# Kernel tuning notes

Measured on AMD Instinct MI355X. Metric: run time of the kernel, lower is better.

Reference implementation:

```python
import jax, jax.numpy as jnp
import numpy as np
from jax import lax

B, L, N = 512, 128, 64      # batch, data_len//2, numOfSmart
H = 16                      # conv channels == lstm hidden
PW = (N - 3) // 2           # pooled width = 30
FEAT = H * PW               # lstm input = 480
BN_EPS = 1e-5


def setup_inputs() -> dict:
    key = jax.random.key(0)
    ks = jax.random.split(key, 24)
    rn = lambda k, shape, s=0.05: jax.random.normal(k, shape, dtype=jnp.float32) * s
    return {
        "input1": jax.random.normal(ks[0], (B, L, N), dtype=jnp.float32),
        "input2": jax.random.normal(ks[1], (B, L, N), dtype=jnp.float32),
        "w_x_q": rn(ks[2], (N, N), 0.1),
        "w_x_k": rn(ks[3], (L, 1), 0.1),
        "w_y_q": rn(ks[4], (L, L), 0.1),
        "w_y_k": rn(ks[5], (1, N), 0.1),
        "pos_emb": rn(ks[6], (L, N), 0.1),
        "conv_w": rn(ks[7], (H, 1, 1, 4), 0.2),
        "conv_b": rn(ks[8], (H,), 0.1),
        "bn_gamma": jnp.ones((H,), jnp.float32),
        "bn_beta": jnp.zeros((H,), jnp.float32),
        "bn_mean": jnp.zeros((H,), jnp.float32),
        "bn_var": jnp.ones((H,), jnp.float32),
        "lstm_Wih0": rn(ks[9], (4 * H, FEAT)),
        "lstm_Whh0": rn(ks[10], (4 * H, H)),
        "lstm_bih0": rn(ks[11], (4 * H,)),
        "lstm_bhh0": rn(ks[12], (4 * H,)),
        "lstm_Wih1": rn(ks[13], (4 * H, H)),
        "lstm_Whh1": rn(ks[14], (4 * H, H)),
        "lstm_bih1": rn(ks[15], (4 * H,)),
        "lstm_bhh1": rn(ks[16], (4 * H,)),
        "fc1_w": rn(ks[17], (8 * L, 16 * L), 0.02),
        "fc1_b": rn(ks[18], (8 * L,), 0.02),
        "fc2_w": rn(ks[19], (8 * L, 8 * L), 0.02),
        "fc2_b": rn(ks[20], (8 * L,), 0.02),
        "fc3_w": rn(ks[21], (20, 8 * L), 0.02),
        "fc3_b": rn(ks[22], (20,), 0.02),
    }


def _lstm_layer(xs, Wih, Whh, bih, bhh):
    # xs: [T, Bt, F]; torch gate order i, f, g, o
    Bt = xs.shape[1]
    h0 = jnp.zeros((Bt, Whh.shape[1]), xs.dtype)

    def step(carry, xt):
        h, c = carry
        g = xt @ Wih.T + h @ Whh.T + bih + bhh
        i, f, gg, o = jnp.split(g, 4, axis=-1)
        c = jax.nn.sigmoid(f) * c + jax.nn.sigmoid(i) * jnp.tanh(gg)
        h = jax.nn.sigmoid(o) * jnp.tanh(c)
        return (h, c), h

    _, ys = lax.scan(step, (h0, h0), xs)
    return ys


def reference(input1, input2, w_x_q, w_x_k, w_y_q, w_y_k, pos_emb, conv_w, conv_b,
              bn_gamma, bn_beta, bn_mean, bn_var,
              lstm_Wih0, lstm_Whh0, lstm_bih0, lstm_bhh0,
              lstm_Wih1, lstm_Whh1, lstm_bih1, lstm_bhh1,
              fc1_w, fc1_b, fc2_w, fc2_b, fc3_w, fc3_b):

    def once(x):  # x: [B, L, N]
        # --- dual-axis attention ---
        x_k = jnp.einsum('bln,lo->bno', x, w_x_k)            # [B,N,1]
        x_q = jnp.einsum('bln,nm->blm', x, w_x_q)            # [B,L,N]
        score_x = jax.nn.softmax(jnp.einsum('bln,bno->blo', x_q, x_k), axis=1) * 10.0  # [B,L,1]
        y_k = jnp.einsum('on,bln->bol', w_y_k, x)            # [B,1,L]
        y_q = jnp.einsum('lm,bmn->bln', w_y_q, x)            # [B,L,N]
        y_ = jnp.einsum('bol,bln->bon', y_k, y_q)[:, 0, :]   # [B,N]
        score_y = jax.nn.softmax(y_, axis=1) * 10.0          # [B,N]
        score_xy = score_x * score_y[:, None, :]             # rank-1 [B,L,N]
        out = x * score_xy + pos_emb                         # pos embedding (arange idx)
        # --- CNN ---
        z = lax.conv_general_dilated(out[:, None], conv_w, (1, 1), 'VALID',
                                     dimension_numbers=('NCHW', 'OIHW', 'NCHW'))
        z = jax.nn.relu(z + conv_b[None, :, None, None])
        scale = (bn_gamma / jnp.sqrt(bn_var + BN_EPS))[None, :, None, None]
        z = (z - bn_mean[None, :, None, None]) * scale + bn_beta[None, :, None, None]
        # maxpool (1,2), floor mode: [B,H,L,61] -> [B,H,L,30]
        w2 = (z.shape[-1] // 2) * 2
        z = z[..., :w2].reshape(z.shape[0], H, L, -1, 2).max(-1)
        # [B,H,L,PW] -> [B,L,H*PW]
        z = jnp.transpose(z, (0, 2, 1, 3)).reshape(z.shape[0], L, FEAT)
        # --- 2-layer LSTM; torch batch_first=False, so scan over axis 0 (=B) ---
        h1 = _lstm_layer(z, lstm_Wih0, lstm_Whh0, lstm_bih0, lstm_bhh0)
        h2 = _lstm_layer(h1, lstm_Wih1, lstm_Whh1, lstm_bih1, lstm_bhh1)  # [B,L,H]
        f = h2.reshape(h2.shape[0], -1)                      # [B, 16*L]
        f = jax.nn.leaky_relu(f @ fc1_w.T + fc1_b, 0.01)
        f = jax.nn.leaky_relu(f @ fc2_w.T + fc2_b, 0.01)
        return f @ fc3_w.T + fc3_b                           # [B, 20]

    return once(input1), once(input2)
```

## Files before the change

kernel.cpp:

```cpp
#include <hip/hip_runtime.h>

#define LSX 65
#define FCS 40

typedef __bf16 bf16x8 __attribute__((ext_vector_type(8)));
typedef float  f32x4  __attribute__((ext_vector_type(4)));

__device__ __forceinline__ unsigned short f2bf_rne(float x) {
    unsigned int u = __float_as_uint(x);
    unsigned int r = u + 0x7FFFu + ((u >> 16) & 1u);
    return (unsigned short)(r >> 16);
}

#define QB(x, C) __uint_as_float((unsigned)__builtin_amdgcn_update_dpp( \
        0, (int)__float_as_uint(x), (C), 0xF, 0xF, false))
#define RDLANE(x, L) __uint_as_float((unsigned)__builtin_amdgcn_readlane( \
        (int)__float_as_uint(x), (L)))

__global__ __launch_bounds__(256) void k_permW(const float* __restrict__ Wih0,
                                               unsigned short* __restrict__ Wfh,
                                               unsigned short* __restrict__ Wfl)
{
    int idx = blockIdx.x * 256 + threadIdx.x;
    int j = idx & 7, lane = (idx >> 3) & 63, nt = (idx >> 9) & 3, ch = idx >> 11;
    int g = nt * 16 + (lane & 15);
    int k = (lane >> 4) * 8 + j;
    int f = ch * 32 + k, q = f >> 4, h = f & 15;
    float v = Wih0[g * 480 + h * 30 + q];
    unsigned int uv = __float_as_uint(v);
    Wfh[idx] = (unsigned short)(uv >> 16);
    Wfl[idx] = f2bf_rne(v - __uint_as_float(uv & 0xFFFF0000u));
}

__global__ __launch_bounds__(256) void k_cvt(const float* __restrict__ in,
                                             unsigned short* __restrict__ oh,
                                             unsigned short* __restrict__ ol,
                                             int n4)
{
    int i = blockIdx.x * 256 + threadIdx.x;
    if (i >= n4) return;
    float4 v = ((const float4*)in)[i];
    float vv[4] = {v.x, v.y, v.z, v.w};
    unsigned short hs[4], ls[4];
    #pragma unroll
    for (int e = 0; e < 4; ++e) {
        unsigned int u = __float_as_uint(vv[e]);
        hs[e] = (unsigned short)(u >> 16);
        ls[e] = f2bf_rne(vv[e] - __uint_as_float(u & 0xFFFF0000u));
    }
    uint2 ph = make_uint2((unsigned)hs[0] | ((unsigned)hs[1] << 16),
                          (unsigned)hs[2] | ((unsigned)hs[3] << 16));
    uint2 pl = make_uint2((unsigned)ls[0] | ((unsigned)ls[1] << 16),
                          (unsigned)ls[2] | ((unsigned)ls[3] << 16));
    *(uint2*)&oh[i * 4] = ph;
    *(uint2*)&ol[i * 4] = pl;
}

__global__ __launch_bounds__(256, 3) void k_attn_conv(
    const float* __restrict__ x1, const float* __restrict__ x2,
    const float* __restrict__ w_x_q, const float* __restrict__ w_x_k,
    const float* __restrict__ w_y_q, const float* __restrict__ w_y_k,
    const float* __restrict__ pos_emb,
    const float* __restrict__ conv_w, const float* __restrict__ conv_b,
    const float* __restrict__ bn_g, const float* __restrict__ bn_b,
    const float* __restrict__ bn_m, const float* __restrict__ bn_v,
    const unsigned short* __restrict__ Wfh, const unsigned short* __restrict__ Wfl,
    float* __restrict__ pre0)
{
    __shared__ float xs[128 * LSX];
    __shared__ float xkp[2][64], ykv[128], uu[64], vv[128];
    __shared__ float sxs[128], sysp[2][64], sys[64];
    __shared__ float cw[16][4], cbs[16], bnsc[16], bnsh[16];

    const int bg = blockIdx.x;
    const int t  = threadIdx.x;
    const float* x = (bg < 512 ? x1 : x2) + (size_t)(bg & 511) * 8192;

    #pragma unroll
    for (int r = 0; r < 32; ++r) {
        int pos = r * 256 + t;
        xs[(pos >> 6) * LSX + (pos & 63)] = x[pos];
    }
    if (t < 16) {
        float sc = bn_g[t] * rsqrtf(bn_v[t] + 1e-5f);
        bnsc[t] = sc;
        bnsh[t] = bn_b[t] - bn_m[t] * sc;
        cbs[t]  = conv_b[t];
        cw[t][0] = conv_w[t * 4 + 0]; cw[t][1] = conv_w[t * 4 + 1];
        cw[t][2] = conv_w[t * 4 + 2]; cw[t][3] = conv_w[t * 4 + 3];
    }
    __syncthreads();

    if (t < 128) {
        int n = t & 63, hf = t >> 6;
        const float* base = &xs[hf * 64 * LSX + n];
        const float* wk = w_x_k + hf * 64;
        float s = 0.f;
        for (int l = 0; l < 64; ++l) s += base[l * LSX] * wk[l];
        xkp[hf][n] = s;
    } else {
        int l = t - 128;
        const float* row = &xs[l * LSX];
        float s = 0.f;
        for (int n = 0; n < 64; ++n) s += w_y_k[n] * row[n];
        ykv[l] = s;
    }
    __syncthreads();

    if (t < 64) {
        const float* wq = w_x_q + t * 64;
        float s = 0.f;
        for (int n = 0; n < 64; ++n) s += wq[n] * (xkp[0][n] + xkp[1][n]);
        uu[t] = s;
    } else if (t < 192) {
        int m = t - 64;
        float s = 0.f;
        for (int l = 0; l < 128; ++l) s += ykv[l] * w_y_q[l * 128 + m];
        vv[m] = s;
    }
    __syncthreads();

    if (t < 128) {
        const float* row = &xs[t * LSX];
        float s = 0.f;
        for (int m = 0; m < 64; ++m) s += row[m] * uu[m];
        sxs[t] = s;
    } else {
        int n = (t - 128) & 63, hf = (t - 128) >> 6;
        const float* base = &xs[hf * 64 * LSX + n];
        const float* vp = vv + hf * 64;
        float s = 0.f;
        for (int m = 0; m < 64; ++m) s += vp[m] * base[m * LSX];
        sysp[hf][n] = s;
    }
    __syncthreads();

    if (t < 64) {
        float a = sxs[t], b = sxs[t + 64];
        float mx = fmaxf(a, b);
        #pragma unroll
        for (int d = 32; d > 0; d >>= 1) mx = fmaxf(mx, __shfl_xor(mx, d, 64));
        float e0 = __expf(a - mx), e1 = __expf(b - mx);
        float s = e0 + e1;
        #pragma unroll
        for (int d = 32; d > 0; d >>= 1) s += __shfl_xor(s, d, 64);
        float r = 10.f / s;
        sxs[t] = e0 * r; sxs[t + 64] = e1 * r;
    } else if (t < 128) {
        int n = t - 64;
        float a = sysp[0][n] + sysp[1][n];
        float mx = a;
        #pragma unroll
        for (int d = 32; d > 0; d >>= 1) mx = fmaxf(mx, __shfl_xor(mx, d, 64));
        float e = __expf(a - mx);
        float s = e;
        #pragma unroll
        for (int d = 32; d > 0; d >>= 1) s += __shfl_xor(s, d, 64);
        sys[n] = e * (10.f / s);
    }
    __syncthreads();

    #pragma unroll
    for (int r = 0; r < 32; ++r) {
        int pos = r * 256 + t;
        int l = pos >> 6, n = pos & 63;
        xs[l * LSX + n] = xs[l * LSX + n] * sxs[l] * sys[n] + pos_emb[pos];
    }
    __syncthreads();

    const int lane = t & 63, w = t >> 6;
    const int m16 = lane & 15, kq = lane >> 4;
    const int hb = (kq & 1) * 8;
    const int qoff = kq >> 1;

    float cwr0[8], cwr1[8], cwr2[8], cwr3[8], cbr[8], bsr[8], bhr[8];
    #pragma unroll
    for (int j = 0; j < 8; ++j) {
        cwr0[j] = cw[hb + j][0]; cwr1[j] = cw[hb + j][1];
        cwr2[j] = cw[hb + j][2]; cwr3[j] = cw[hb + j][3];
        cbr[j] = cbs[hb + j]; bsr[j] = bnsc[hb + j]; bhr[j] = bnsh[hb + j];
    }

    f32x4 acc[2][4];
    #pragma unroll
    for (int mt = 0; mt < 2; ++mt)
        #pragma unroll
        for (int nt = 0; nt < 4; ++nt) {
            f32x4 z = {0.f, 0.f, 0.f, 0.f};
            acc[mt][nt] = z;
        }

    for (int ch = 0; ch < 15; ++ch) {
        bf16x8 bh[4], bl[4];
        #pragma unroll
        for (int nt = 0; nt < 4; ++nt) {
            int o = ((ch * 4 + nt) * 64 + lane) * 8;
            bh[nt] = *(const bf16x8*)&Wfh[o];
            bl[nt] = *(const bf16x8*)&Wfl[o];
        }
        bf16x8 ah[2], al[2];
        const int q2 = 2 * (2 * ch + qoff);
        #pragma unroll
        for (int mt = 0; mt < 2; ++mt) {
            int row = w * 32 + mt * 16 + m16;
            const float* xr = &xs[row * LSX + q2];
            float o0 = xr[0], o1 = xr[1], o2 = xr[2], o3 = xr[3], o4 = xr[4];
            union { unsigned short us[8]; bf16x8 bv; } vh, vl;
            #pragma unroll
            for (int j = 0; j < 8; ++j) {
                float a = fmaf(o0, cwr0[j], fmaf(o1, cwr1[j], fmaf(o2, cwr2[j], fmaf(o3, cwr3[j], cbr[j]))));
                float b = fmaf(o1, cwr0[j], fmaf(o2, cwr1[j], fmaf(o3, cwr2[j], fmaf(o4, cwr3[j], cbr[j]))));
                a = fmaf(fmaxf(a, 0.f), bsr[j], bhr[j]);
                b = fmaf(fmaxf(b, 0.f), bsr[j], bhr[j]);
                float v = fmaxf(a, b);
                unsigned int uv = __float_as_uint(v);
                vh.us[j] = (unsigned short)(uv >> 16);
                vl.us[j] = f2bf_rne(v - __uint_as_float(uv & 0xFFFF0000u));
            }
            ah[mt] = vh.bv; al[mt] = vl.bv;
        }
        #pragma unroll
        for (int mt = 0; mt < 2; ++mt)
            #pragma unroll
            for (int nt = 0; nt < 4; ++nt) {
                acc[mt][nt] = __builtin_amdgcn_mfma_f32_16x16x32_bf16(ah[mt], bh[nt], acc[mt][nt], 0, 0, 0);
                acc[mt][nt] = __builtin_amdgcn_mfma_f32_16x16x32_bf16(al[mt], bh[nt], acc[mt][nt], 0, 0, 0);
                acc[mt][nt] = __builtin_amdgcn_mfma_f32_16x16x32_bf16(ah[mt], bl[nt], acc[mt][nt], 0, 0, 0);
            }
    }

    #pragma unroll
    for (int mt = 0; mt < 2; ++mt)
        #pragma unroll
        for (int nt = 0; nt < 4; ++nt)
            #pragma unroll
            for (int r = 0; r < 4; ++r) {
                int row = w * 32 + mt * 16 + (lane >> 4) * 4 + r;
                int col = nt * 16 + m16;
                pre0[(size_t)bg * 8192 + row * 64 + col] = acc[mt][nt][r];
            }
}

__global__ __launch_bounds__(128) void k_lstm(
    const float* __restrict__ pre0,
    const float* __restrict__ Whh0,
    const float* __restrict__ Wih1, const float* __restrict__ Whh1,
    const float* __restrict__ bih0, const float* __restrict__ bhh0,
    const float* __restrict__ bih1, const float* __restrict__ bhh1,
    unsigned short* __restrict__ fbh, unsigned short* __restrict__ fbl)
{
    __shared__ float zbuf[2][8][64];

    const int blk = blockIdx.x;
    const int i = blk >> 7, j = blk & 127;
    const int tid = threadIdx.x;
    const int lane = tid & 63;
    const int wv = tid >> 6;
    const int a = lane & 3, u = lane >> 2;
    const int row = a * 16 + u;
    const float pm = (a == 2) ? -2.f : -1.f;
    const float ka = (a == 2) ?  2.f :  1.f;
    const float kb = (a == 2) ? -1.f :  0.f;

    if (wv == 0) {
        float w0[16], wi1[16];
        #pragma unroll
        for (int m = 0; m < 16; ++m) {
            w0[m]  = Whh0[row * 16 + m];
            wi1[m] = Wih1[row * 16 + m];
        }
        const float b0 = bih0[row] + bhh0[row];
        float h0[16];
        #pragma unroll
        for (int m = 0; m < 16; ++m) h0[m] = 0.f;
        float c0 = 0.f;

        const float* pp = pre0 + (size_t)i * 4194304 + (size_t)j * 64 + row;
        float pf[8];
        #pragma unroll
        for (int d = 0; d < 8; ++d) pf[d] = pp[(size_t)d * 8192];

#define STEP0(PRE, DD, BB)                                                      \
    {                                                                           \
        float sA = 0.f, sB = 0.f, sC = 0.f, sD = 0.f;                           \
        _Pragma("unroll")                                                       \
        for (int m = 0; m < 4; ++m) {                                           \
            sA += h0[m]      * w0[m];                                           \
            sB += h0[m + 4]  * w0[m + 4];                                       \
            sC += h0[m + 8]  * w0[m + 8];                                       \
            sD += h0[m + 12] * w0[m + 12];                                      \
        }                                                                       \
        float g0 = (PRE) + b0 + ((sA + sB) + (sC + sD));                        \
        float e0 = __expf(pm * g0);                                             \
        float v0 = fmaf(__builtin_amdgcn_rcpf(1.f + e0), ka, kb);               \
        float si = QB(v0, 0x00), sf = QB(v0, 0x55);                             \
        float tg = QB(v0, 0xAA), so = QB(v0, 0xFF);                             \
        c0 = fmaf(sf, c0, si * tg);                                             \
        float ec = __expf(-2.f * c0);                                           \
        float h0n = so * fmaf(2.f, __builtin_amdgcn_rcpf(1.f + ec), -1.f);      \
        float hn[16];                                                           \
        _Pragma("unroll")                                                       \
        for (int m = 0; m < 16; ++m) hn[m] = RDLANE(h0n, 4 * m);                \
        float zA = 0.f, zB = 0.f, zC = 0.f, zD = 0.f;                           \
        _Pragma("unroll")                                                       \
        for (int m = 0; m < 4; ++m) {                                           \
            zA += hn[m]      * wi1[m];                                          \
            zB += hn[m + 4]  * wi1[m + 4];                                      \
            zC += hn[m + 8]  * wi1[m + 8];                                      \
            zD += hn[m + 12] * wi1[m + 12];                                     \
        }                                                                       \
        zbuf[BB][DD][lane] = (zA + zB) + (zC + zD);                             \
        _Pragma("unroll")                                                       \
        for (int m = 0; m < 16; ++m) h0[m] = hn[m];                             \
    }

        for (int tb = 0; tb < 64; ++tb) {
            const int bb = tb & 1;
            float nx[8];
            #pragma unroll
            for (int d = 0; d < 8; ++d)
                nx[d] = pp[(size_t)(tb * 8 + 8 + d) * 8192];
            STEP0(pf[0], 0, bb);
            STEP0(pf[1], 1, bb);
            STEP0(pf[2], 2, bb);
            STEP0(pf[3], 3, bb);
            STEP0(pf[4], 4, bb);
            STEP0(pf[5], 5, bb);
            STEP0(pf[6], 6, bb);
            STEP0(pf[7], 7, bb);
            #pragma unroll
            for (int d = 0; d < 8; ++d) pf[d] = nx[d];
            __syncthreads();
        }
        __syncthreads();
#undef STEP0
    } else {
        float wh1[16];
        #pragma unroll
        for (int m = 0; m < 16; ++m) wh1[m] = Whh1[row * 16 + m];
        const float b1 = bih1[row] + bhh1[row];
        float h1[16];
        #pragma unroll
        for (int m = 0; m < 16; ++m) h1[m] = 0.f;
        float c1 = 0.f;

        const size_t fbase = (size_t)i * 1048576 + (size_t)j * 16 + u;
        const bool st = (a == 0);

#define STEP1(ZZ, TT)                                                           \
    {                                                                           \
        float tA = 0.f, tB = 0.f, tC = 0.f, tD = 0.f;                           \
        _Pragma("unroll")                                                       \
        for (int m = 0; m < 4; ++m) {                                           \
            tA += h1[m]      * wh1[m];                                          \
            tB += h1[m + 4]  * wh1[m + 4];                                      \
            tC += h1[m + 8]  * wh1[m + 8];                                      \
            tD += h1[m + 12] * wh1[m + 12];                                     \
        }                                                                       \
        float g1 = (ZZ) + b1 + ((tA + tB) + (tC + tD));                         \
        float e1 = __expf(pm * g1);                                             \
        float v1 = fmaf(__builtin_amdgcn_rcpf(1.f + e1), ka, kb);               \
        float si1 = QB(v1, 0x00), sf1 = QB(v1, 0x55);                           \
        float tg1 = QB(v1, 0xAA), so1 = QB(v1, 0xFF);                           \
        c1 = fmaf(sf1, c1, si1 * tg1);                                          \
        float ec1 = __expf(-2.f * c1);                                          \
        float h1n = so1 * fmaf(2.f, __builtin_amdgcn_rcpf(1.f + ec1), -1.f);    \
        if (st) {                                                               \
            unsigned int uh = __float_as_uint(h1n);                             \
            fbh[fbase + (size_t)(TT) * 2048] = (unsigned short)(uh >> 16);      \
            fbl[fbase + (size_t)(TT) * 2048] =                                  \
                f2bf_rne(h1n - __uint_as_float(uh & 0xFFFF0000u));              \
        }                                                                       \
        _Pragma("unroll")                                                       \
        for (int m = 0; m < 16; ++m) h1[m] = RDLANE(h1n, 4 * m);                \
    }

        __syncthreads();
        for (int tb = 0; tb < 64; ++tb) {
            const int bb = tb & 1;
            float zz[8];
            #pragma unroll
            for (int d = 0; d < 8; ++d) zz[d] = zbuf[bb][d][lane];
            const int t0 = tb * 8;
            STEP1(zz[0], t0 + 0);
            STEP1(zz[1], t0 + 1);
            STEP1(zz[2], t0 + 2);
            STEP1(zz[3], t0 + 3);
            STEP1(zz[4], t0 + 4);
            STEP1(zz[5], t0 + 5);
            STEP1(zz[6], t0 + 6);
            STEP1(zz[7], t0 + 7);
            __syncthreads();
        }
#undef STEP1
    }
}

__global__ __launch_bounds__(256) void k_fcmm(
    const unsigned short* __restrict__ Ahg, const unsigned short* __restrict__ Alg,
    const unsigned short* __restrict__ Bhg, const unsigned short* __restrict__ Blg,
    const float* __restrict__ bias,
    float* __restrict__ Cf, unsigned short* __restrict__ Chh,
    unsigned short* __restrict__ Chl,
    int N, int K)
{
    __shared__ unsigned short Ah[64 * FCS], Al[64 * FCS];
    __shared__ unsigned short Bh[64 * FCS], Bl[64 * FCS];
    const int t = threadIdx.x;
    const int lane = t & 63, w = t >> 6;
    const int wr = (w >> 1) * 32, wc = (w & 1) * 32;
    const int m0 = blockIdx.y * 64, n0 = blockIdx.x * 64;
    const int m16 = lane & 15, kb = (lane >> 4) * 8;
    const int sr = t >> 2, skg = (t & 3) * 8;

    f32x4 acc[2][2];
    #pragma unroll
    for (int mt = 0; mt < 2; ++mt)
        #pragma unroll
        for (int nt = 0; nt < 2; ++nt) {
            f32x4 z = {0.f, 0.f, 0.f, 0.f};
            acc[mt][nt] = z;
        }

    for (int kc = 0; kc < K; kc += 32) {
        size_t ga = (size_t)(m0 + sr) * K + kc + skg;
        size_t gb = (size_t)(n0 + sr) * K + kc + skg;
        *(uint4*)&Ah[sr * FCS + skg] = *(const uint4*)&Ahg[ga];
        *(uint4*)&Al[sr * FCS + skg] = *(const uint4*)&Alg[ga];
        *(uint4*)&Bh[sr * FCS + skg] = *(const uint4*)&Bhg[gb];
        *(uint4*)&Bl[sr * FCS + skg] = *(const uint4*)&Blg[gb];
        __syncthreads();

        bf16x8 afh[2], afl[2], bfh[2], bfl[2];
        #pragma unroll
        for (int mt = 0; mt < 2; ++mt) {
            int off = (wr + mt * 16 + m16) * FCS + kb;
            afh[mt] = *(const bf16x8*)&Ah[off];
            afl[mt] = *(const bf16x8*)&Al[off];
        }
        #pragma unroll
        for (int nt = 0; nt < 2; ++nt) {
            int off = (wc + nt * 16 + m16) * FCS + kb;
            bfh[nt] = *(const bf16x8*)&Bh[off];
            bfl[nt] = *(const bf16x8*)&Bl[off];
        }
        #pragma unroll
        for (int mt = 0; mt < 2; ++mt)
            #pragma unroll
            for (int nt = 0; nt < 2; ++nt) {
                acc[mt][nt] = __builtin_amdgcn_mfma_f32_16x16x32_bf16(afh[mt], bfh[nt], acc[mt][nt], 0, 0, 0);
                acc[mt][nt] = __builtin_amdgcn_mfma_f32_16x16x32_bf16(afl[mt], bfh[nt], acc[mt][nt], 0, 0, 0);
                acc[mt][nt] = __builtin_amdgcn_mfma_f32_16x16x32_bf16(afh[mt], bfl[nt], acc[mt][nt], 0, 0, 0);
            }
        __syncthreads();
    }

    #pragma unroll
    for (int mt = 0; mt < 2; ++mt)
        #pragma unroll
        for (int nt = 0; nt < 2; ++nt)
            #pragma unroll
            for (int r = 0; r < 4; ++r) {
                int rr = m0 + wr + mt * 16 + (lane >> 4) * 4 + r;
                int cc = n0 + wc + nt * 16 + m16;
                float v = acc[mt][nt][r] + bias[cc];
                v = (v > 0.f) ? v : 0.01f * v;
                if (Cf) {
                    Cf[(size_t)rr * N + cc] = v;
                } else {
                    unsigned int uv = __float_as_uint(v);
                    Chh[(size_t)rr * N + cc] = (unsigned short)(uv >> 16);
                    Chl[(size_t)rr * N + cc] =
                        f2bf_rne(v - __uint_as_float(uv & 0xFFFF0000u));
                }
            }
}

__global__ __launch_bounds__(256) void k_fc3(
    const float* __restrict__ A, const float* __restrict__ W,
    const float* __restrict__ bias, float* __restrict__ out)
{
    __shared__ float row[1024];
    __shared__ float red[20][8];
    const int m = blockIdx.x;
    const int t = threadIdx.x;
    #pragma unroll
    for (int r = 0; r < 4; ++r) row[r * 256 + t] = A[(size_t)m * 1024 + r * 256 + t];
    __syncthreads();
    if (t < 160) {
        int o = t >> 3, seg = t & 7;
        const float* w = W + (size_t)o * 1024 + seg * 128;
        const float* rr = &row[seg * 128];
        float s = 0.f;
        for (int kk = 0; kk < 128; ++kk) s += rr[kk] * w[kk];
        red[o][seg] = s;
    }
    __syncthreads();
    if (t < 20) {
        float s = bias[t];
        #pragma unroll
        for (int seg = 0; seg < 8; ++seg) s += red[t][seg];
        out[(size_t)m * 20 + t] = s;
    }
}

extern "C" void kernel_launch(void* const* d_in, const int* in_sizes, int n_in,
                              void* d_out, int out_size, void* d_ws, size_t ws_size,
                              hipStream_t stream) {
    const float* in1    = (const float*)d_in[0];
    const float* in2    = (const float*)d_in[1];
    const float* w_x_q  = (const float*)d_in[2];
    const float* w_x_k  = (const float*)d_in[3];
    const float* w_y_q  = (const float*)d_in[4];
    const float* w_y_k  = (const float*)d_in[5];
    const float* posemb = (const float*)d_in[6];
    const float* conv_w = (const float*)d_in[7];
    const float* conv_b = (const float*)d_in[8];
    const float* bn_g   = (const float*)d_in[9];
    const float* bn_b   = (const float*)d_in[10];
    const float* bn_m   = (const float*)d_in[11];
    const float* bn_v   = (const float*)d_in[12];
    const float* Wih0   = (const float*)d_in[13];
    const float* Whh0   = (const float*)d_in[14];
    const float* bih0   = (const float*)d_in[15];
    const float* bhh0   = (const float*)d_in[16];
    const float* Wih1   = (const float*)d_in[17];
    const float* Whh1   = (const float*)d_in[18];
    const float* bih1   = (const float*)d_in[19];
    const float* bhh1   = (const float*)d_in[20];
    const float* fc1w   = (const float*)d_in[21];
    const float* fc1b   = (const float*)d_in[22];
    const float* fc2w   = (const float*)d_in[23];
    const float* fc2b   = (const float*)d_in[24];
    const float* fc3w   = (const float*)d_in[25];
    const float* fc3b   = (const float*)d_in[26];
    float* out = (float*)d_out;

    float* ws = (float*)d_ws;
    float* pre0            = ws;
    unsigned short* fbh    = (unsigned short*)(ws + 8466432);
    unsigned short* fbl    = (unsigned short*)(ws + 9515008);
    unsigned short* f1h    = (unsigned short*)(ws + 10563584);
    unsigned short* f1l    = (unsigned short*)(ws + 11087872);
    float* f2              = ws + 11612160;
    unsigned short* w1h    = (unsigned short*)(ws + 12660736);
    unsigned short* w1l    = (unsigned short*)(ws + 13709312);
    unsigned short* w2h    = (unsigned short*)(ws + 14757888);
    unsigned short* w2l    = (unsigned short*)(ws + 15282176);
    unsigned short* Wfh    = (unsigned short*)(ws + 15806464);
    unsigned short* Wfl    = (unsigned short*)(ws + 15821824);

    k_permW<<<120, 256, 0, stream>>>(Wih0, Wfh, Wfl);
    k_cvt<<<2048, 256, 0, stream>>>(fc1w, w1h, w1l, 524288);
    k_cvt<<<1024, 256, 0, stream>>>(fc2w, w2h, w2l, 262144);
    k_attn_conv<<<1024, 256, 0, stream>>>(in1, in2, w_x_q, w_x_k, w_y_q, w_y_k,
                                          posemb, conv_w, conv_b, bn_g, bn_b,
                                          bn_m, bn_v, Wfh, Wfl, pre0);
    k_lstm<<<256, 128, 0, stream>>>(pre0, Whh0, Wih1, Whh1,
                                    bih0, bhh0, bih1, bhh1, fbh, fbl);
    dim3 gfc(16, 16);
    k_fcmm<<<gfc, 256, 0, stream>>>(fbh, fbl, w1h, w1l, fc1b,
                                    nullptr, f1h, f1l, 1024, 2048);
    k_fcmm<<<gfc, 256, 0, stream>>>(f1h, f1l, w2h, w2l, fc2b,
                                    f2, nullptr, nullptr, 1024, 1024);
    k_fc3<<<1024, 256, 0, stream>>>(f2, fc3w, fc3b, out);
}
```

Before: 237.4 us.

## Interleave two independent LSTM recurrences per block and split attention reductions

The LSTM kernel now runs both inputs' recurrences (previously separate blocks) inside one block. Their dependent chains are interleaved, which hides the latency of exp/rcp/readlane along the sequential scan, and the grid is halved to 128 blocks. The attention reductions also use four partial accumulators to break the serial FMA dependency. The cost is fewer blocks running in parallel, more register pressure, and a slightly different float summation order.

```diff
diff --git a/kernel.cpp b/kernel.cpp
--- a/kernel.cpp
+++ b/kernel.cpp
@@ -95,43 +95,73 @@
         int n = t & 63, hf = t >> 6;
         const float* base = &xs[hf * 64 * LSX + n];
         const float* wk = w_x_k + hf * 64;
-        float s = 0.f;
-        for (int l = 0; l < 64; ++l) s += base[l * LSX] * wk[l];
-        xkp[hf][n] = s;
+        float s0 = 0.f, s1 = 0.f, s2 = 0.f, s3 = 0.f;
+        for (int l = 0; l < 64; l += 4) {
+            s0 += base[(l + 0) * LSX] * wk[l + 0];
+            s1 += base[(l + 1) * LSX] * wk[l + 1];
+            s2 += base[(l + 2) * LSX] * wk[l + 2];
+            s3 += base[(l + 3) * LSX] * wk[l + 3];
+        }
+        xkp[hf][n] = (s0 + s1) + (s2 + s3);
     } else {
         int l = t - 128;
         const float* row = &xs[l * LSX];
-        float s = 0.f;
-        for (int n = 0; n < 64; ++n) s += w_y_k[n] * row[n];
-        ykv[l] = s;
+        float s0 = 0.f, s1 = 0.f, s2 = 0.f, s3 = 0.f;
+        for (int n = 0; n < 64; n += 4) {
+            s0 += w_y_k[n + 0] * row[n + 0];
+            s1 += w_y_k[n + 1] * row[n + 1];
+            s2 += w_y_k[n + 2] * row[n + 2];
+            s3 += w_y_k[n + 3] * row[n + 3];
+        }
+        ykv[l] = (s0 + s1) + (s2 + s3);
     }
     __syncthreads();
 
     if (t < 64) {
         const float* wq = w_x_q + t * 64;
-        float s = 0.f;
-        for (int n = 0; n < 64; ++n) s += wq[n] * (xkp[0][n] + xkp[1][n]);
-        uu[t] = s;
+        float s0 = 0.f, s1 = 0.f, s2 = 0.f, s3 = 0.f;
+        for (int n = 0; n < 64; n += 4) {
+            s0 += wq[n + 0] * (xkp[0][n + 0] + xkp[1][n + 0]);
+            s1 += wq[n + 1] * (xkp[0][n + 1] + xkp[1][n + 1]);
+            s2 += wq[n + 2] * (xkp[0][n + 2] + xkp[1][n + 2]);
+            s3 += wq[n + 3] * (xkp[0][n + 3] + xkp[1][n + 3]);
+        }
+        uu[t] = (s0 + s1) + (s2 + s3);
     } else if (t < 192) {
         int m = t - 64;
-        float s = 0.f;
-        for (int l = 0; l < 128; ++l) s += ykv[l] * w_y_q[l * 128 + m];
-        vv[m] = s;
+        float s0 = 0.f, s1 = 0.f, s2 = 0.f, s3 = 0.f;
+        for (int l = 0; l < 128; l += 4) {
+            s0 += ykv[l + 0] * w_y_q[(l + 0) * 128 + m];
+            s1 += ykv[l + 1] * w_y_q[(l + 1) * 128 + m];
+            s2 += ykv[l + 2] * w_y_q[(l + 2) * 128 + m];
+            s3 += ykv[l + 3] * w_y_q[(l + 3) * 128 + m];
+        }
+        vv[m] = (s0 + s1) + (s2 + s3);
     }
     __syncthreads();
 
     if (t < 128) {
         const float* row = &xs[t * LSX];
-        float s = 0.f;
-        for (int m = 0; m < 64; ++m) s += row[m] * uu[m];
-        sxs[t] = s;
+        float s0 = 0.f, s1 = 0.f, s2 = 0.f, s3 = 0.f;
+        for (int m = 0; m < 64; m += 4) {
+            s0 += row[m + 0] * uu[m + 0];
+            s1 += row[m + 1] * uu[m + 1];
+            s2 += row[m + 2] * uu[m + 2];
+            s3 += row[m + 3] * uu[m + 3];
+        }
+        sxs[t] = (s0 + s1) + (s2 + s3);
     } else {
         int n = (t - 128) & 63, hf = (t - 128) >> 6;
         const float* base = &xs[hf * 64 * LSX + n];
         const float* vp = vv + hf * 64;
-        float s = 0.f;
-        for (int m = 0; m < 64; ++m) s += vp[m] * base[m * LSX];
-        sysp[hf][n] = s;
+        float s0 = 0.f, s1 = 0.f, s2 = 0.f, s3 = 0.f;
+        for (int m = 0; m < 64; m += 4) {
+            s0 += vp[m + 0] * base[(m + 0) * LSX];
+            s1 += vp[m + 1] * base[(m + 1) * LSX];
+            s2 += vp[m + 2] * base[(m + 2) * LSX];
+            s3 += vp[m + 3] * base[(m + 3) * LSX];
+        }
+        sysp[hf][n] = (s0 + s1) + (s2 + s3);
     }
     __syncthreads();
 
@@ -249,10 +279,10 @@
     const float* __restrict__ bih1, const float* __restrict__ bhh1,
     unsigned short* __restrict__ fbh, unsigned short* __restrict__ fbl)
 {
-    __shared__ float zbuf[2][8][64];
-
-    const int blk = blockIdx.x;
-    const int i = blk >> 7, j = blk & 127;
+    __shared__ float zbA[2][8][64];
+    __shared__ float zbB[2][8][64];
+
+    const int j = blockIdx.x;
     const int tid = threadIdx.x;
     const int lane = tid & 63;
     const int wv = tid >> 6;
@@ -270,129 +300,166 @@
             wi1[m] = Wih1[row * 16 + m];
         }
         const float b0 = bih0[row] + bhh0[row];
-        float h0[16];
-        #pragma unroll
-        for (int m = 0; m < 16; ++m) h0[m] = 0.f;
-        float c0 = 0.f;
-
-        const float* pp = pre0 + (size_t)i * 4194304 + (size_t)j * 64 + row;
-        float pf[8];
-        #pragma unroll
-        for (int d = 0; d < 8; ++d) pf[d] = pp[(size_t)d * 8192];
-
-#define STEP0(PRE, DD, BB)                                                      \
+        float hA[16], hB[16];
+        #pragma unroll
+        for (int m = 0; m < 16; ++m) { hA[m] = 0.f; hB[m] = 0.f; }
+        float cA = 0.f, cB = 0.f;
+
+        const float* ppA = pre0 + (size_t)j * 64 + row;
+        const float* ppB = ppA + 4194304;
+        float pfA[8], pfB[8];
+        #pragma unroll
+        for (int d = 0; d < 8; ++d) {
+            pfA[d] = ppA[(size_t)d * 8192];
+            pfB[d] = ppB[(size_t)d * 8192];
+        }
+
+#define STEP0P(PA, PB, DD, BB)                                                  \
     {                                                                           \
-        float sA = 0.f, sB = 0.f, sC = 0.f, sD = 0.f;                           \
+        float sA0 = 0.f, sA1 = 0.f, sA2 = 0.f, sA3 = 0.f;                       \
+        float sB0 = 0.f, sB1 = 0.f, sB2 = 0.f, sB3 = 0.f;                       \
         _Pragma("unroll")                                                       \
         for (int m = 0; m < 4; ++m) {                                           \
-            sA += h0[m]      * w0[m];                                           \
-            sB += h0[m + 4]  * w0[m + 4];                                       \
-            sC += h0[m + 8]  * w0[m + 8];                                       \
-            sD += h0[m + 12] * w0[m + 12];                                      \
+            sA0 += hA[m]      * w0[m];      sB0 += hB[m]      * w0[m];          \
+            sA1 += hA[m + 4]  * w0[m + 4];  sB1 += hB[m + 4]  * w0[m + 4];      \
+            sA2 += hA[m + 8]  * w0[m + 8];  sB2 += hB[m + 8]  * w0[m + 8];      \
+            sA3 += hA[m + 12] * w0[m + 12]; sB3 += hB[m + 12] * w0[m + 12];     \
         }                                                                       \
-        float g0 = (PRE) + b0 + ((sA + sB) + (sC + sD));                        \
-        float e0 = __expf(pm * g0);                                             \
-        float v0 = fmaf(__builtin_amdgcn_rcpf(1.f + e0), ka, kb);               \
-        float si = QB(v0, 0x00), sf = QB(v0, 0x55);                             \
-        float tg = QB(v0, 0xAA), so = QB(v0, 0xFF);                             \
-        c0 = fmaf(sf, c0, si * tg);                                             \
-        float ec = __expf(-2.f * c0);                                           \
-        float h0n = so * fmaf(2.f, __builtin_amdgcn_rcpf(1.f + ec), -1.f);      \
-        float hn[16];                                                           \
+        float gA = (PA) + b0 + ((sA0 + sA1) + (sA2 + sA3));                     \
+        float gB = (PB) + b0 + ((sB0 + sB1) + (sB2 + sB3));                     \
+        float eA = __expf(pm * gA);                                             \
+        float eB = __expf(pm * gB);                                             \
+        float vA = fmaf(__builtin_amdgcn_rcpf(1.f + eA), ka, kb);               \
+        float vB = fmaf(__builtin_amdgcn_rcpf(1.f + eB), ka, kb);               \
+        float siA = QB(vA, 0x00), sfA = QB(vA, 0x55);                           \
+        float siB = QB(vB, 0x00), sfB = QB(vB, 0x55);                           \
+        float tgA = QB(vA, 0xAA), soA = QB(vA, 0xFF);                           \
+        float tgB = QB(vB, 0xAA), soB = QB(vB, 0xFF);                           \
+        cA = fmaf(sfA, cA, siA * tgA);                                          \
+        cB = fmaf(sfB, cB, siB * tgB);                                          \
+        float ecA = __expf(-2.f * cA);                                          \
+        float ecB = __expf(-2.f * cB);                                          \
+        float hAn = soA * fmaf(2.f, __builtin_amdgcn_rcpf(1.f + ecA), -1.f);    \
+        float hBn = soB * fmaf(2.f, __builtin_amdgcn_rcpf(1.f + ecB), -1.f);    \
         _Pragma("unroll")                                                       \
-        for (int m = 0; m < 16; ++m) hn[m] = RDLANE(h0n, 4 * m);                \
-        float zA = 0.f, zB = 0.f, zC = 0.f, zD = 0.f;                           \
+        for (int m = 0; m < 16; ++m) {                                          \
+            hA[m] = RDLANE(hAn, 4 * m);                                         \
+            hB[m] = RDLANE(hBn, 4 * m);                                         \
+        }                                                                       \
+        float zA0 = 0.f, zA1 = 0.f, zA2 = 0.f, zA3 = 0.f;                       \
+        float zB0 = 0.f, zB1 = 0.f, zB2 = 0.f, zB3 = 0.f;                       \
         _Pragma("unroll")                                                       \
         for (int m = 0; m < 4; ++m) {                                           \
-            zA += hn[m]      * wi1[m];                                          \
-            zB += hn[m + 4]  * wi1[m + 4];                                      \
-            zC += hn[m + 8]  * wi1[m + 8];                                      \
-            zD += hn[m + 12] * wi1[m + 12];                                     \
+            zA0 += hA[m]      * wi1[m];      zB0 += hB[m]      * wi1[m];        \
+            zA1 += hA[m + 4]  * wi1[m + 4];  zB1 += hB[m + 4]  * wi1[m + 4];    \
+            zA2 += hA[m + 8]  * wi1[m + 8];  zB2 += hB[m + 8]  * wi1[m + 8];    \
+            zA3 += hA[m + 12] * wi1[m + 12]; zB3 += hB[m + 12] * wi1[m + 12];   \
         }                                                                       \
-        zbuf[BB][DD][lane] = (zA + zB) + (zC + zD);                             \
-        _Pragma("unroll")                                                       \
-        for (int m = 0; m < 16; ++m) h0[m] = hn[m];                             \
+        zbA[BB][DD][lane] = (zA0 + zA1) + (zA2 + zA3);                          \
+        zbB[BB][DD][lane] = (zB0 + zB1) + (zB2 + zB3);                          \
     }
 
         for (int tb = 0; tb < 64; ++tb) {
             const int bb = tb & 1;
-            float nx[8];
-            #pragma unroll
-            for (int d = 0; d < 8; ++d)
-                nx[d] = pp[(size_t)(tb * 8 + 8 + d) * 8192];
-            STEP0(pf[0], 0, bb);
-            STEP0(pf[1], 1, bb);
-            STEP0(pf[2], 2, bb);
-            STEP0(pf[3], 3, bb);
-            STEP0(pf[4], 4, bb);
-            STEP0(pf[5], 5, bb);
-            STEP0(pf[6], 6, bb);
-            STEP0(pf[7], 7, bb);
-            #pragma unroll
-            for (int d = 0; d < 8; ++d) pf[d] = nx[d];
+            float nxA[8], nxB[8];
+            #pragma unroll
+            for (int d = 0; d < 8; ++d) {
+                nxA[d] = ppA[(size_t)(tb * 8 + 8 + d) * 8192];
+                nxB[d] = ppB[(size_t)(tb * 8 + 8 + d) * 8192];
+            }
+            STEP0P(pfA[0], pfB[0], 0, bb);
+            STEP0P(pfA[1], pfB[1], 1, bb);
+            STEP0P(pfA[2], pfB[2], 2, bb);
+            STEP0P(pfA[3], pfB[3], 3, bb);
+            STEP0P(pfA[4], pfB[4], 4, bb);
+            STEP0P(pfA[5], pfB[5], 5, bb);
+            STEP0P(pfA[6], pfB[6], 6, bb);
+            STEP0P(pfA[7], pfB[7], 7, bb);
+            #pragma unroll
+            for (int d = 0; d < 8; ++d) { pfA[d] = nxA[d]; pfB[d] = nxB[d]; }
             __syncthreads();
         }
         __syncthreads();
-#undef STEP0
+#undef STEP0P
     } else {
         float wh1[16];
         #pragma unroll
         for (int m = 0; m < 16; ++m) wh1[m] = Whh1[row * 16 + m];
         const float b1 = bih1[row] + bhh1[row];
-        float h1[16];
-        #pragma unroll
-        for (int m = 0; m < 16; ++m) h1[m] = 0.f;
-        float c1 = 0.f;
-
-        const size_t fbase = (size_t)i * 1048576 + (size_t)j * 16 + u;
+        float h1A[16], h1B[16];
+        #pragma unroll
+        for (int m = 0; m < 16; ++m) { h1A[m] = 0.f; h1B[m] = 0.f; }
+        float c1A = 0.f, c1B = 0.f;
+
+        const size_t fbaseA = (size_t)j * 16 + u;
+        const size_t fbaseB = fbaseA + 1048576;
         const bool st = (a == 0);
 
-#define STEP1(ZZ, TT)                                                           \
+#define STEP1P(ZA, ZB, TT)                                                      \
     {                                                                           \
-        float tA = 0.f, tB = 0.f, tC = 0.f, tD = 0.f;                           \
+        float tA0 = 0.f, tA1 = 0.f, tA2 = 0.f, tA3 = 0.f;                       \
+        float tB0 = 0.f, tB1 = 0.f, tB2 = 0.f, tB3 = 0.f;                       \
         _Pragma("unroll")                                                       \
         for (int m = 0; m < 4; ++m) {                                           \
-            tA += h1[m]      * wh1[m];                                          \
-            tB += h1[m + 4]  * wh1[m + 4];                                      \
-            tC += h1[m + 8]  * wh1[m + 8];                                      \
-            tD += h1[m + 12] * wh1[m + 12];                                     \
+            tA0 += h1A[m]      * wh1[m];      tB0 += h1B[m]      * wh1[m];      \
+            tA1 += h1A[m + 4]  * wh1[m + 4];  tB1 += h1B[m + 4]  * wh1[m + 4];  \
+            tA2 += h1A[m + 8]  * wh1[m + 8];  tB2 += h1B[m + 8]  * wh1[m + 8];  \
+            tA3 += h1A[m + 12] * wh1[m + 12]; tB3 += h1B[m + 12] * wh1[m + 12]; \
         }                                                                       \
-        float g1 = (ZZ) + b1 + ((tA + tB) + (tC + tD));                         \
-        float e1 = __expf(pm * g1);                                             \
-        float v1 = fmaf(__builtin_amdgcn_rcpf(1.f + e1), ka, kb);               \
-        float si1 = QB(v1, 0x00), sf1 = QB(v1, 0x55);                           \
-        float tg1 = QB(v1, 0xAA), so1 = QB(v1, 0xFF);                           \
-        c1 = fmaf(sf1, c1, si1 * tg1);                                          \
-        float ec1 = __expf(-2.f * c1);                                          \
-        float h1n = so1 * fmaf(2.f, __builtin_amdgcn_rcpf(1.f + ec1), -1.f);    \
+        float gA = (ZA) + b1 + ((tA0 + tA1) + (tA2 + tA3));                     \
+        float gB = (ZB) + b1 + ((tB0 + tB1) + (tB2 + tB3));                     \
+        float eA = __expf(pm * gA);                                             \
+        float eB = __expf(pm * gB);                                             \
+        float vA = fmaf(__builtin_amdgcn_rcpf(1.f + eA), ka, kb);               \
+        float vB = fmaf(__builtin_amdgcn_rcpf(1.f + eB), ka, kb);               \
+        float siA = QB(vA, 0x00), sfA = QB(vA, 0x55);                           \
+        float siB = QB(vB, 0x00), sfB = QB(vB, 0x55);                           \
+        float tgA = QB(vA, 0xAA), soA = QB(vA, 0xFF);                           \
+        float tgB = QB(vB, 0xAA), soB = QB(vB, 0xFF);                           \
+        c1A = fmaf(sfA, c1A, siA * tgA);                                        \
+        c1B = fmaf(sfB, c1B, siB * tgB);                                        \
+        float ecA = __expf(-2.f * c1A);                                         \
+        float ecB = __expf(-2.f * c1B);                                         \
+        float hAn = soA * fmaf(2.f, __builtin_amdgcn_rcpf(1.f + ecA), -1.f);    \
+        float hBn = soB * fmaf(2.f, __builtin_amdgcn_rcpf(1.f + ecB), -1.f);    \
         if (st) {                                                               \
-            unsigned int uh = __float_as_uint(h1n);                             \
-            fbh[fbase + (size_t)(TT) * 2048] = (unsigned short)(uh >> 16);      \
-            fbl[fbase + (size_t)(TT) * 2048] =                                  \
-                f2bf_rne(h1n - __uint_as_float(uh & 0xFFFF0000u));              \
+            unsigned int uA = __float_as_uint(hAn);                             \
+            unsigned int uB = __float_as_uint(hBn);                             \
+            fbh[fbaseA + (size_t)(TT) * 2048] = (unsigned short)(uA >> 16);     \
+            fbh[fbaseB + (size_t)(TT) * 2048] = (unsigned short)(uB >> 16);     \
+            fbl[fbaseA + (size_t)(TT) * 2048] =                                 \
+                f2bf_rne(hAn - __uint_as_float(uA & 0xFFFF0000u));              \
+            fbl[fbaseB + (size_t)(TT) * 2048] =                                 \
+                f2bf_rne(hBn - __uint_as_float(uB & 0xFFFF0000u));              \
         }                                                                       \
         _Pragma("unroll")                                                       \
-        for (int m = 0; m < 16; ++m) h1[m] = RDLANE(h1n, 4 * m);                \
+        for (int m = 0; m < 16; ++m) {                                          \
+            h1A[m] = RDLANE(hAn, 4 * m);                                        \
+            h1B[m] = RDLANE(hBn, 4 * m);                                        \
+        }                                                                       \
     }
 
         __syncthreads();
         for (int tb = 0; tb < 64; ++tb) {
             const int bb = tb & 1;
-            float zz[8];
-            #pragma unroll
-            for (int d = 0; d < 8; ++d) zz[d] = zbuf[bb][d][lane];
+            float zzA[8], zzB[8];
+            #pragma unroll
+            for (int d = 0; d < 8; ++d) {
+                zzA[d] = zbA[bb][d][lane];
+                zzB[d] = zbB[bb][d][lane];
+            }
             const int t0 = tb * 8;
-            STEP1(zz[0], t0 + 0);
-            STEP1(zz[1], t0 + 1);
-            STEP1(zz[2], t0 + 2);
-            STEP1(zz[3], t0 + 3);
-            STEP1(zz[4], t0 + 4);
-            STEP1(zz[5], t0 + 5);
-            STEP1(zz[6], t0 + 6);
-            STEP1(zz[7], t0 + 7);
+            STEP1P(zzA[0], zzB[0], t0 + 0);
+            STEP1P(zzA[1], zzB[1], t0 + 1);
+            STEP1P(zzA[2], zzB[2], t0 + 2);
+            STEP1P(zzA[3], zzB[3], t0 + 3);
+            STEP1P(zzA[4], zzB[4], t0 + 4);
+            STEP1P(zzA[5], zzB[5], t0 + 5);
+            STEP1P(zzA[6], zzB[6], t0 + 6);
+            STEP1P(zzA[7], zzB[7], t0 + 7);
             __syncthreads();
         }
-#undef STEP1
+#undef STEP1P
     }
 }
 
@@ -556,7 +623,7 @@
     k_attn_conv<<<1024, 256, 0, stream>>>(in1, in2, w_x_q, w_x_k, w_y_q, w_y_k,
                                           posemb, conv_w, conv_b, bn_g, bn_b,
                                           bn_m, bn_v, Wfh, Wfl, pre0);
-    k_lstm<<<256, 128, 0, stream>>>(pre0, Whh0, Wih1, Whh1,
+    k_lstm<<<128, 128, 0, stream>>>(pre0, Whh0, Wih1, Whh1,
                                     bih0, bhh0, bih1, bhh1, fbh, fbl);
     dim3 gfc(16, 16);
     k_fcmm<<<gfc, 256, 0, stream>>>(fbh, fbl, w1h, w1l, fc1b,
```

New measurement: 302.1 us. 27.3% more time.
